# Kernel tuning notes

Measured on AMD Instinct MI355X. Metric: run time of the kernel, lower is better.

## Reference

```python
import jax, jax.numpy as jnp
import numpy as np

B, N_SERIES, T, HIDDEN = 256, 512, 512, 1024
EPS = 1e-5  # BatchNorm1d default eps


def setup_inputs() -> dict:
    key = jax.random.key(0)
    ks = jax.random.split(key, 6)
    s_in = 1.0 / np.sqrt(N_SERIES)
    s_hid = 1.0 / np.sqrt(2 * HIDDEN)
    s_out = 1.0 / np.sqrt(HIDDEN)
    return {
        "x": jax.random.normal(ks[0], (B, N_SERIES, T), dtype=jnp.float32),
        # input_layer: Linear(n_series -> hidden)
        "Wi": jax.random.uniform(ks[1], (HIDDEN, N_SERIES), jnp.float32, -s_in, s_in),
        "bi": jnp.zeros((HIDDEN,), jnp.float32),
        # hidden_layer: Linear(2*hidden -> hidden)
        "Wh": jax.random.uniform(ks[2], (HIDDEN, 2 * HIDDEN), jnp.float32, -s_hid, s_hid),
        "bh": jnp.zeros((HIDDEN,), jnp.float32),
        # BatchNorm1d(hidden) affine params
        "gamma": jnp.ones((HIDDEN,), jnp.float32),
        "beta": jnp.zeros((HIDDEN,), jnp.float32),
        # last_layer: Linear(hidden -> n_series)
        "Wl": jax.random.uniform(ks[3], (N_SERIES, HIDDEN), jnp.float32, -s_out, s_out),
        "bl": jnp.zeros((N_SERIES,), jnp.float32),
    }


def reference(x, Wi, bi, Wh, bh, gamma, beta, Wl, bl):
    # x: [B, n_series, T] -> time-major [T, B, n_series]
    xt = jnp.transpose(x, (2, 0, 1))
    h0 = jnp.zeros((x.shape[0], Wh.shape[0]), x.dtype)

    def step(h, x_t):
        inp = x_t @ Wi.T + bi                              # [B, H]
        emb = jnp.concatenate([inp, h], axis=1)            # [B, 2H]
        h_new = jnp.tanh(emb @ Wh.T + bh)                  # [B, H]
        return h_new, None

    hidden, _ = jax.lax.scan(step, h0, xt)
    # BatchNorm1d, training-mode batch statistics (biased variance)
    mean = jnp.mean(hidden, axis=0)
    var = jnp.var(hidden, axis=0)
    h_bn = gamma * (hidden - mean) / jnp.sqrt(var + EPS) + beta
    return h_bn @ Wl.T + bl                                # [B, n_series]
```

## Files before the change

kernel.cpp:

```cpp
#include <hip/hip_runtime.h>

typedef _Float16 f16;
typedef _Float16 half8 __attribute__((ext_vector_type(8)));
typedef float f32x4 __attribute__((ext_vector_type(4)));

#define HIDDEN 1024
#define NSER 512
#define BATCH 256
#define TSTEPS 512

__device__ __forceinline__ float tanh_fast(float x) {
  x = fminf(15.0f, fmaxf(-15.0f, x));
  float e = __expf(2.0f * x);
  return (e - 1.0f) / (e + 1.0f);
}


__global__ __launch_bounds__(256) void convert_whl_kernel(const float* __restrict__ Wh,
                                                          f16* __restrict__ WhLh) {
  int idx = blockIdx.x * 256 + threadIdx.x;
  int j = idx >> 10, k = idx & 1023;
  WhLh[idx] = (f16)Wh[((size_t)j << 11) + k];
}

__global__ __launch_bounds__(256) void convert_wl_kernel(const float* __restrict__ Wl,
                                                         f16* __restrict__ Wlh) {
  int idx = blockIdx.x * 256 + threadIdx.x;
  Wlh[idx] = (f16)Wl[idx];
}

__global__ __launch_bounds__(256) void transpose_wi_kernel(const float* __restrict__ Wi,
                                                           f16* __restrict__ WiT) {
  __shared__ float tile[32][33];
  int tx = threadIdx.x & 31, ty = threadIdx.x >> 5;
  int c0 = blockIdx.x * 32;
  int r0 = blockIdx.y * 32;
#pragma unroll
  for (int i = 0; i < 32; i += 8)
    tile[ty + i][tx] = Wi[(size_t)(r0 + ty + i) * NSER + c0 + tx];
  __syncthreads();
#pragma unroll
  for (int i = 0; i < 32; i += 8)
    WiT[(size_t)(c0 + ty + i) * HIDDEN + r0 + tx] = (f16)tile[tx][ty + i];
}

__global__ __launch_bounds__(256) void transpose_x_kernel(const float* __restrict__ x,
                                                          f16* __restrict__ xT) {
  __shared__ float tile[32][33];
  int b = blockIdx.z;
  int t0 = blockIdx.x * 32, n0 = blockIdx.y * 32;
  int tx = threadIdx.x & 31, ty = threadIdx.x >> 5;
#pragma unroll
  for (int i = 0; i < 32; i += 8)
    tile[ty + i][tx] = x[((size_t)b * NSER + n0 + ty + i) * TSTEPS + t0 + tx];
  __syncthreads();
#pragma unroll
  for (int i = 0; i < 32; i += 8)
    xT[((size_t)(t0 + ty + i) * BATCH + b) * NSER + n0 + tx] = (f16)tile[tx][ty + i];
}

__global__ __launch_bounds__(256) void beff_kernel(const float* __restrict__ Wh,
                                                   const float* __restrict__ bi,
                                                   const float* __restrict__ bh,
                                                   float* __restrict__ beff) {
  __shared__ float red[256];
  int j = blockIdx.x;
  float s = 0.f;
  for (int k = threadIdx.x; k < HIDDEN; k += 256)
    s += Wh[(size_t)j * 2048 + k] * bi[k];
  red[threadIdx.x] = s;
  __syncthreads();
  for (int off = 128; off > 0; off >>= 1) {
    if (threadIdx.x < (unsigned)off) red[threadIdx.x] += red[threadIdx.x + off];
    __syncthreads();
  }
  if (threadIdx.x == 0) beff[j] = bh[j] + red[0];
}

template <bool OUT_F16, bool HAS_BIAS>
__global__ __launch_bounds__(256) void gemm_f16_kernel(const f16* __restrict__ A,
                                                       const f16* __restrict__ B,
                                                       const float* __restrict__ bias,
                                                       void* __restrict__ Cp,
                                                       int M, int N, int K) {
  (void)M;
  __shared__ f16 As[128 * 64];
  __shared__ f16 Bs[128 * 64];
  const int tid = threadIdx.x;
  const int l = tid & 63, w = tid >> 6;
  const int wr = w >> 1, wc = w & 1;
  const int lr = l & 15, lg = l >> 4;
  const size_t m0 = (size_t)blockIdx.y * 128, n0 = (size_t)blockIdx.x * 128;
  f32x4 acc[4][4] = {};
  for (int k0 = 0; k0 < K; k0 += 64) {
    half8 ar[4], br[4];
#pragma unroll
    for (int c = 0; c < 4; ++c) {
      int Gq = c * 256 + tid;
      int row = Gq >> 3, colg = Gq & 7;
      ar[c] = *(const half8*)&A[(m0 + row) * K + k0 + colg * 8];
      br[c] = *(const half8*)&B[(n0 + row) * K + k0 + colg * 8];
    }
    __syncthreads();
#pragma unroll
    for (int c = 0; c < 4; ++c) {
      int Gq = c * 256 + tid;
      *(half8*)&As[Gq * 8] = ar[c];
      *(half8*)&Bs[Gq * 8] = br[c];
    }
    __syncthreads();
#pragma unroll
    for (int ks = 0; ks < 2; ++ks) {
      half8 a[4], b[4];
#pragma unroll
      for (int i = 0; i < 4; ++i)
        a[i] = *(const half8*)&As[(wr * 64 + i * 16 + lr) * 64 + ks * 32 + lg * 8];
#pragma unroll
      for (int i = 0; i < 4; ++i)
        b[i] = *(const half8*)&Bs[(wc * 64 + i * 16 + lr) * 64 + ks * 32 + lg * 8];
#pragma unroll
      for (int mi = 0; mi < 4; ++mi)
#pragma unroll
        for (int ni = 0; ni < 4; ++ni)
          acc[mi][ni] = __builtin_amdgcn_mfma_f32_16x16x32_f16(a[mi], b[ni], acc[mi][ni], 0, 0, 0);
    }
  }
#pragma unroll
  for (int mi = 0; mi < 4; ++mi) {
#pragma unroll
    for (int ni = 0; ni < 4; ++ni) {
      size_t n = n0 + wc * 64 + ni * 16 + lr;
      float bv = 0.f;
      if constexpr (HAS_BIAS) bv = bias[n];
#pragma unroll
      for (int r = 0; r < 4; ++r) {
        size_t m = m0 + wr * 64 + mi * 16 + lg * 4 + r;
        float v = acc[mi][ni][r] + bv;
        if constexpr (OUT_F16)
          ((f16*)Cp)[m * (size_t)N + n] = (f16)v;
        else
          ((float*)Cp)[m * (size_t)N + n] = v;
      }
    }
  }
}

__global__ __launch_bounds__(512) void rnn_kernel(const float* __restrict__ Wh,
                                                  const f16* __restrict__ Z,
                                                  f16* hb0, f16* hb1,
                                                  float* __restrict__ h_final,
                                                  unsigned int* canary) {
  const int bid = blockIdx.x;
  const int g = bid >> 3, q = bid & 7;
  const int tid = threadIdx.x;
  const int l = tid & 63, w = tid >> 6;
  const int lr = l & 15, lg = l >> 4;
  const int b0 = g * 16;
  const int jcol = q * 128 + w * 16 + lr;

  half8 breg[32];
#pragma unroll
  for (int ks = 0; ks < 32; ++ks) {
    const float* s = &Wh[(size_t)jcol * 2048 + HIDDEN + ks * 32 + lg * 8];
    half8 hv;
#pragma unroll
    for (int i = 0; i < 8; ++i) hv[i] = (f16)s[i];
    breg[ks] = hv;
  }

  __shared__ f16 hs[16 * HIDDEN];

  for (int t = 0; t < TSTEPS; ++t) {
    const f16* hprev = (t & 1) ? hb1 : hb0;
    f16* hnext = (t & 1) ? hb0 : hb1;

    const f16* zp = &Z[((size_t)t * BATCH + b0 + lg * 4) * HIDDEN + jcol];
    f16 z0 = zp[0], z1 = zp[HIDDEN], z2 = zp[2 * HIDDEN], z3 = zp[3 * HIDDEN];

    {
      const unsigned* cp = &canary[g * 8 + (l & 7)];
      unsigned cv;
      int guard = 0;
      do {
        asm volatile("global_load_dword %0, %1, off sc0 sc1\n\ts_waitcnt vmcnt(0)"
                     : "=v"(cv)
                     : "v"(cp)
                     : "memory");
      } while (__ballot(cv < (unsigned)t) != 0ull && ++guard < (1 << 20));
    }

    half8 hv[4];
#pragma unroll
    for (int i = 0; i < 4; ++i) {
      int G = i * 512 + tid;
      int row = G >> 7, gI = G & 127;
      const f16* src = &hprev[(size_t)(b0 + row) * HIDDEN + gI * 8];
      asm volatile("global_load_dwordx4 %0, %1, off sc0 sc1" : "=v"(hv[i]) : "v"(src));
    }
    asm volatile("s_waitcnt vmcnt(0)" ::: "memory");

#pragma unroll
    for (int i = 0; i < 4; ++i) {
      int G = i * 512 + tid;
      int row = G >> 7, gI = G & 127;
      *(half8*)&hs[row * HIDDEN + ((gI ^ (row & 7)) * 8)] = hv[i];
    }
    __syncthreads();

    f32x4 acc0 = {0.f, 0.f, 0.f, 0.f}, acc1 = acc0, acc2 = acc0, acc3 = acc0;
#pragma unroll
    for (int ks = 0; ks < 32; ks += 4) {
      int gA0 = ks * 4 + lg;
      half8 a0 = *(const half8*)&hs[lr * HIDDEN + ((gA0 ^ (lr & 7)) * 8)];
      half8 a1 = *(const half8*)&hs[lr * HIDDEN + (((gA0 + 4) ^ (lr & 7)) * 8)];
      half8 a2 = *(const half8*)&hs[lr * HIDDEN + (((gA0 + 8) ^ (lr & 7)) * 8)];
      half8 a3 = *(const half8*)&hs[lr * HIDDEN + (((gA0 + 12) ^ (lr & 7)) * 8)];
      acc0 = __builtin_amdgcn_mfma_f32_16x16x32_f16(a0, breg[ks + 0], acc0, 0, 0, 0);
      acc1 = __builtin_amdgcn_mfma_f32_16x16x32_f16(a1, breg[ks + 1], acc1, 0, 0, 0);
      acc2 = __builtin_amdgcn_mfma_f32_16x16x32_f16(a2, breg[ks + 2], acc2, 0, 0, 0);
      acc3 = __builtin_amdgcn_mfma_f32_16x16x32_f16(a3, breg[ks + 3], acc3, 0, 0, 0);
    }
    f32x4 acc = (acc0 + acc1) + (acc2 + acc3);

    float v0 = tanh_fast(acc[0] + (float)z0);
    float v1 = tanh_fast(acc[1] + (float)z1);
    float v2 = tanh_fast(acc[2] + (float)z2);
    float v3 = tanh_fast(acc[3] + (float)z3);

    if (t == TSTEPS - 1) {
      h_final[(size_t)(b0 + lg * 4 + 0) * HIDDEN + jcol] = v0;
      h_final[(size_t)(b0 + lg * 4 + 1) * HIDDEN + jcol] = v1;
      h_final[(size_t)(b0 + lg * 4 + 2) * HIDDEN + jcol] = v2;
      h_final[(size_t)(b0 + lg * 4 + 3) * HIDDEN + jcol] = v3;
    } else {
      unsigned s0 = (unsigned)__builtin_bit_cast(unsigned short, (f16)v0);
      unsigned s1 = (unsigned)__builtin_bit_cast(unsigned short, (f16)v1);
      unsigned s2 = (unsigned)__builtin_bit_cast(unsigned short, (f16)v2);
      unsigned s3 = (unsigned)__builtin_bit_cast(unsigned short, (f16)v3);
      f16* p0 = &hnext[(size_t)(b0 + lg * 4 + 0) * HIDDEN + jcol];
      asm volatile("global_store_short %0, %1, off sc0 sc1" ::"v"(p0), "v"(s0) : "memory");
      asm volatile("global_store_short %0, %1, off sc0 sc1" ::"v"(p0 + HIDDEN), "v"(s1) : "memory");
      asm volatile("global_store_short %0, %1, off sc0 sc1" ::"v"(p0 + 2 * HIDDEN), "v"(s2) : "memory");
      asm volatile("global_store_short %0, %1, off sc0 sc1" ::"v"(p0 + 3 * HIDDEN), "v"(s3) : "memory");
      asm volatile("s_waitcnt vmcnt(0)" ::: "memory");
      __syncthreads();
      if (tid == 0) {
        unsigned nv = (unsigned)(t + 1);
        asm volatile("global_store_dword %0, %1, off sc0 sc1" ::"v"(&canary[g * 8 + q]),
                     "v"(nv)
                     : "memory");
      }
    }
  }
}

__global__ __launch_bounds__(256) void bn_kernel(const float* __restrict__ hf,
                                                 const float* __restrict__ gamma,
                                                 const float* __restrict__ beta,
                                                 f16* __restrict__ hbn) {
  int j = blockIdx.x * 256 + threadIdx.x;
  float s1 = 0.f, s2 = 0.f;
  for (int b = 0; b < BATCH; ++b) {
    float v = hf[(size_t)b * HIDDEN + j];
    s1 += v;
    s2 += v * v;
  }
  float mean = s1 * (1.f / BATCH);
  float var = s2 * (1.f / BATCH) - mean * mean;
  float sc = gamma[j] * rsqrtf(var + 1e-5f);
  float sh = beta[j] - mean * sc;
  for (int b = 0; b < BATCH; ++b)
    hbn[(size_t)b * HIDDEN + j] = (f16)(hf[(size_t)b * HIDDEN + j] * sc + sh);
}

extern "C" void kernel_launch(void* const* d_in, const int* in_sizes, int n_in,
                              void* d_out, int out_size, void* d_ws, size_t ws_size,
                              hipStream_t stream) {
  (void)in_sizes; (void)n_in; (void)out_size;
  const float* x     = (const float*)d_in[0];
  const float* Wi    = (const float*)d_in[1];
  const float* bi    = (const float*)d_in[2];
  const float* Wh    = (const float*)d_in[3];
  const float* bh    = (const float*)d_in[4];
  const float* gamma = (const float*)d_in[5];
  const float* beta  = (const float*)d_in[6];
  const float* Wl    = (const float*)d_in[7];
  const float* bl    = (const float*)d_in[8];
  float* out = (float*)d_out;

  char* wsp = (char*)d_ws;
  size_t off = 0;
  auto alloc = [&](size_t bytes) -> void* {
    void* p = (void*)(wsp + off);
    off += (bytes + 255) & ~(size_t)255;
    return p;
  };
  f16*      Zb    = (f16*)alloc((size_t)TSTEPS * BATCH * HIDDEN * 2);
  f16*      xT    = (f16*)alloc((size_t)TSTEPS * BATCH * NSER * 2);
  f16*      WhLh  = (f16*)alloc((size_t)HIDDEN * HIDDEN * 2);
  f16*      WiT   = (f16*)alloc((size_t)NSER * HIDDEN * 2);
  f16*      Wlh   = (f16*)alloc((size_t)NSER * HIDDEN * 2);
  f16*      Weff  = (f16*)alloc((size_t)HIDDEN * NSER * 2);
  float*    beff  = (float*)alloc(HIDDEN * 4);
  f16*      hbuf0 = (f16*)alloc((size_t)BATCH * HIDDEN * 2);
  f16*      hbuf1 = (f16*)alloc((size_t)BATCH * HIDDEN * 2);
  float*    hfin  = (float*)alloc((size_t)BATCH * HIDDEN * 4);
  f16*      hbn   = (f16*)alloc((size_t)BATCH * HIDDEN * 2);
  unsigned* canary = (unsigned*)alloc(16 * 8 * 4);
  if (off > ws_size) return;

  hipMemsetAsync(canary, 0, 16 * 8 * 4, stream);
  hipMemsetAsync(hbuf0, 0, (size_t)BATCH * HIDDEN * 2, stream);

  convert_whl_kernel<<<4096, 256, 0, stream>>>(Wh, WhLh);
  transpose_wi_kernel<<<dim3(16, 32), 256, 0, stream>>>(Wi, WiT);
  convert_wl_kernel<<<2048, 256, 0, stream>>>(Wl, Wlh);
  beff_kernel<<<1024, 256, 0, stream>>>(Wh, bi, bh, beff);
  gemm_f16_kernel<true, false><<<dim3(4, 8), 256, 0, stream>>>(WhLh, WiT, nullptr, Weff,
                                                               1024, NSER, HIDDEN);
  transpose_x_kernel<<<dim3(16, 16, 256), 256, 0, stream>>>(x, xT);
  gemm_f16_kernel<true, true><<<dim3(8, 1024), 256, 0, stream>>>(xT, Weff, beff, Zb,
                                                                 TSTEPS * BATCH, HIDDEN, NSER);
  rnn_kernel<<<128, 512, 0, stream>>>(Wh, Zb, hbuf0, hbuf1, hfin, canary);
  bn_kernel<<<4, 256, 0, stream>>>(hfin, gamma, beta, hbn);
  gemm_f16_kernel<false, true><<<dim3(4, 2), 256, 0, stream>>>(hbn, Wlh, bl, out,
                                                               BATCH, NSER, HIDDEN);
}
```

Before: 2.794 ms.

## Replace canary flag sync with tagged-data mailboxes in persistent RNN kernel

Each hidden-state value is now written as a 32-bit word carrying the fp16 value plus a timestep tag, so consumers poll the data itself instead of spinning on a separate canary counter and then reloading h. This removes the store-drain, the block barrier and the flag-write round trip on every step, and also prefetches the next step's Z values during the current step. In exchange the mailbox traffic doubles in size, the spin loop rereads the full 16-row tile on each miss, and it relies on 32-bit stores being seen whole.

```diff
diff --git a/kernel.cpp b/kernel.cpp
--- a/kernel.cpp
+++ b/kernel.cpp
@@ -3,6 +3,8 @@
 typedef _Float16 f16;
 typedef _Float16 half8 __attribute__((ext_vector_type(8)));
 typedef float f32x4 __attribute__((ext_vector_type(4)));
+typedef unsigned int u32x4 __attribute__((ext_vector_type(4)));
+typedef unsigned int u32x2 __attribute__((ext_vector_type(2)));
 
 #define HIDDEN 1024
 #define NSER 512
@@ -145,11 +147,10 @@
   }
 }
 
-__global__ __launch_bounds__(512) void rnn_kernel(const float* __restrict__ Wh,
-                                                  const f16* __restrict__ Z,
-                                                  f16* hb0, f16* hb1,
-                                                  float* __restrict__ h_final,
-                                                  unsigned int* canary) {
+__global__ __launch_bounds__(512, 2) void rnn_kernel(const float* __restrict__ Wh,
+                                                     const f16* __restrict__ Z,
+                                                     unsigned* mb0, unsigned* mb1,
+                                                     float* __restrict__ h_final) {
   const int bid = blockIdx.x;
   const int g = bid >> 3, q = bid & 7;
   const int tid = threadIdx.x;
@@ -158,6 +159,9 @@
   const int b0 = g * 16;
   const int jcol = q * 128 + w * 16 + lr;
 
+  const int u = tid & 255;
+  const int rb = tid >> 8;
+
   half8 breg[32];
 #pragma unroll
   for (int ks = 0; ks < 32; ++ks) {
@@ -170,42 +174,71 @@
 
   __shared__ f16 hs[16 * HIDDEN];
 
-  for (int t = 0; t < TSTEPS; ++t) {
-    const f16* hprev = (t & 1) ? hb1 : hb0;
-    f16* hnext = (t & 1) ? hb0 : hb1;
-
-    const f16* zp = &Z[((size_t)t * BATCH + b0 + lg * 4) * HIDDEN + jcol];
-    f16 z0 = zp[0], z1 = zp[HIDDEN], z2 = zp[2 * HIDDEN], z3 = zp[3 * HIDDEN];
-
+  __builtin_amdgcn_sched_barrier(0);
+  asm volatile("s_waitcnt vmcnt(0)" ::: "memory");
+
+  unsigned zA[4], zB[4];
+  {
+    const f16* zp = &Z[((size_t)0 * BATCH + b0 + lg * 4) * HIDDEN + jcol];
+#pragma unroll
+    for (int r = 0; r < 4; ++r)
+      asm volatile("global_load_ushort %0, %1, off" : "=v"(zA[r]) : "v"(zp + r * HIDDEN));
+  }
+
+  auto step = [&](int t, unsigned (&zc)[4], unsigned (&zn)[4]) {
+    const unsigned* mbr = (t & 1) ? mb1 : mb0;
+    unsigned* mbw = (t & 1) ? mb0 : mb1;
+
+    u32x4 hv[8];
+#pragma unroll
+    for (int i = 0; i < 8; ++i) {
+      const unsigned* src = mbr + (size_t)(b0 + i * 2 + rb) * HIDDEN + u * 4;
+      asm volatile("global_load_dwordx4 %0, %1, off sc0 sc1" : "=v"(hv[i]) : "v"(src));
+    }
     {
-      const unsigned* cp = &canary[g * 8 + (l & 7)];
-      unsigned cv;
-      int guard = 0;
-      do {
-        asm volatile("global_load_dword %0, %1, off sc0 sc1\n\ts_waitcnt vmcnt(0)"
-                     : "=v"(cv)
-                     : "v"(cp)
-                     : "memory");
-      } while (__ballot(cv < (unsigned)t) != 0ull && ++guard < (1 << 20));
-    }
-
-    half8 hv[4];
-#pragma unroll
-    for (int i = 0; i < 4; ++i) {
-      int G = i * 512 + tid;
-      int row = G >> 7, gI = G & 127;
-      const f16* src = &hprev[(size_t)(b0 + row) * HIDDEN + gI * 8];
-      asm volatile("global_load_dwordx4 %0, %1, off sc0 sc1" : "=v"(hv[i]) : "v"(src));
-    }
-    asm volatile("s_waitcnt vmcnt(0)" ::: "memory");
-
-#pragma unroll
-    for (int i = 0; i < 4; ++i) {
-      int G = i * 512 + tid;
-      int row = G >> 7, gI = G & 127;
-      *(half8*)&hs[row * HIDDEN + ((gI ^ (row & 7)) * 8)] = hv[i];
-    }
-    __syncthreads();
+      int tp = (t + 1 < TSTEPS) ? t + 1 : TSTEPS - 1;
+      const f16* zp = &Z[((size_t)tp * BATCH + b0 + lg * 4) * HIDDEN + jcol];
+#pragma unroll
+      for (int r = 0; r < 4; ++r)
+        asm volatile("global_load_ushort %0, %1, off" : "=v"(zn[r]) : "v"(zp + r * HIDDEN));
+    }
+    asm volatile("s_waitcnt vmcnt(4)" ::: "memory");
+
+    const unsigned texp = (unsigned)t << 16;
+    int tries = 0;
+    while (true) {
+      unsigned bad = 0;
+#pragma unroll
+      for (int i = 0; i < 8; ++i) {
+        bad |= hv[i][0] ^ texp;
+        bad |= hv[i][1] ^ texp;
+        bad |= hv[i][2] ^ texp;
+        bad |= hv[i][3] ^ texp;
+      }
+      if (__ballot((bad >> 16) != 0u) == 0ull) break;
+      if (++tries > (1 << 18)) break;
+#pragma unroll
+      for (int i = 0; i < 8; ++i) {
+        const unsigned* src = mbr + (size_t)(b0 + i * 2 + rb) * HIDDEN + u * 4;
+        asm volatile("global_load_dwordx4 %0, %1, off sc0 sc1" : "=v"(hv[i]) : "v"(src));
+      }
+      asm volatile("s_waitcnt vmcnt(0)" ::: "memory");
+    }
+
+#pragma unroll
+    for (int i = 0; i < 8; ++i) {
+      asm volatile("" : "+v"(hv[i]));
+      unsigned p0 = (hv[i][0] & 0xffffu) | (hv[i][1] << 16);
+      unsigned p1 = (hv[i][2] & 0xffffu) | (hv[i][3] << 16);
+      int row = i * 2 + rb;
+      int gI = u >> 1, half = u & 1;
+      u32x2 pv = {p0, p1};
+      *(u32x2*)((char*)hs + row * 2048 + ((gI ^ (row & 7)) * 16) + half * 8) = pv;
+    }
+    asm volatile("s_waitcnt lgkmcnt(0)" ::: "memory");
+    __builtin_amdgcn_sched_barrier(0);
+    __builtin_amdgcn_s_barrier();
+    __builtin_amdgcn_sched_barrier(0);
 
     f32x4 acc0 = {0.f, 0.f, 0.f, 0.f}, acc1 = acc0, acc2 = acc0, acc3 = acc0;
 #pragma unroll
@@ -222,10 +255,12 @@
     }
     f32x4 acc = (acc0 + acc1) + (acc2 + acc3);
 
-    float v0 = tanh_fast(acc[0] + (float)z0);
-    float v1 = tanh_fast(acc[1] + (float)z1);
-    float v2 = tanh_fast(acc[2] + (float)z2);
-    float v3 = tanh_fast(acc[3] + (float)z3);
+#pragma unroll
+    for (int r = 0; r < 4; ++r) asm volatile("" : "+v"(zc[r]));
+    float v0 = tanh_fast(acc[0] + (float)__builtin_bit_cast(f16, (unsigned short)zc[0]));
+    float v1 = tanh_fast(acc[1] + (float)__builtin_bit_cast(f16, (unsigned short)zc[1]));
+    float v2 = tanh_fast(acc[2] + (float)__builtin_bit_cast(f16, (unsigned short)zc[2]));
+    float v3 = tanh_fast(acc[3] + (float)__builtin_bit_cast(f16, (unsigned short)zc[3]));
 
     if (t == TSTEPS - 1) {
       h_final[(size_t)(b0 + lg * 4 + 0) * HIDDEN + jcol] = v0;
@@ -233,24 +268,25 @@
       h_final[(size_t)(b0 + lg * 4 + 2) * HIDDEN + jcol] = v2;
       h_final[(size_t)(b0 + lg * 4 + 3) * HIDDEN + jcol] = v3;
     } else {
-      unsigned s0 = (unsigned)__builtin_bit_cast(unsigned short, (f16)v0);
-      unsigned s1 = (unsigned)__builtin_bit_cast(unsigned short, (f16)v1);
-      unsigned s2 = (unsigned)__builtin_bit_cast(unsigned short, (f16)v2);
-      unsigned s3 = (unsigned)__builtin_bit_cast(unsigned short, (f16)v3);
-      f16* p0 = &hnext[(size_t)(b0 + lg * 4 + 0) * HIDDEN + jcol];
-      asm volatile("global_store_short %0, %1, off sc0 sc1" ::"v"(p0), "v"(s0) : "memory");
-      asm volatile("global_store_short %0, %1, off sc0 sc1" ::"v"(p0 + HIDDEN), "v"(s1) : "memory");
-      asm volatile("global_store_short %0, %1, off sc0 sc1" ::"v"(p0 + 2 * HIDDEN), "v"(s2) : "memory");
-      asm volatile("global_store_short %0, %1, off sc0 sc1" ::"v"(p0 + 3 * HIDDEN), "v"(s3) : "memory");
-      asm volatile("s_waitcnt vmcnt(0)" ::: "memory");
-      __syncthreads();
-      if (tid == 0) {
-        unsigned nv = (unsigned)(t + 1);
-        asm volatile("global_store_dword %0, %1, off sc0 sc1" ::"v"(&canary[g * 8 + q]),
-                     "v"(nv)
-                     : "memory");
-      }
-    }
+      const unsigned tag = (unsigned)(t + 1) << 16;
+      unsigned d0 = (unsigned)__builtin_bit_cast(unsigned short, (f16)v0) | tag;
+      unsigned d1 = (unsigned)__builtin_bit_cast(unsigned short, (f16)v1) | tag;
+      unsigned d2 = (unsigned)__builtin_bit_cast(unsigned short, (f16)v2) | tag;
+      unsigned d3 = (unsigned)__builtin_bit_cast(unsigned short, (f16)v3) | tag;
+      unsigned* p0 = mbw + (size_t)(b0 + lg * 4) * HIDDEN + jcol;
+      asm volatile("global_store_dword %0, %1, off sc0 sc1" ::"v"(p0), "v"(d0) : "memory");
+      asm volatile("global_store_dword %0, %1, off sc0 sc1" ::"v"(p0 + HIDDEN), "v"(d1) : "memory");
+      asm volatile("global_store_dword %0, %1, off sc0 sc1" ::"v"(p0 + 2 * HIDDEN), "v"(d2) : "memory");
+      asm volatile("global_store_dword %0, %1, off sc0 sc1" ::"v"(p0 + 3 * HIDDEN), "v"(d3) : "memory");
+    }
+    __builtin_amdgcn_sched_barrier(0);
+    __builtin_amdgcn_s_barrier();
+    __builtin_amdgcn_sched_barrier(0);
+  };
+
+  for (int t = 0; t < TSTEPS; t += 2) {
+    step(t, zA, zB);
+    step(t + 1, zB, zA);
   }
 }
 
@@ -302,15 +338,14 @@
   f16*      Wlh   = (f16*)alloc((size_t)NSER * HIDDEN * 2);
   f16*      Weff  = (f16*)alloc((size_t)HIDDEN * NSER * 2);
   float*    beff  = (float*)alloc(HIDDEN * 4);
-  f16*      hbuf0 = (f16*)alloc((size_t)BATCH * HIDDEN * 2);
-  f16*      hbuf1 = (f16*)alloc((size_t)BATCH * HIDDEN * 2);
+  unsigned* mb0   = (unsigned*)alloc((size_t)BATCH * HIDDEN * 4);
+  unsigned* mb1   = (unsigned*)alloc((size_t)BATCH * HIDDEN * 4);
   float*    hfin  = (float*)alloc((size_t)BATCH * HIDDEN * 4);
   f16*      hbn   = (f16*)alloc((size_t)BATCH * HIDDEN * 2);
-  unsigned* canary = (unsigned*)alloc(16 * 8 * 4);
   if (off > ws_size) return;
 
-  hipMemsetAsync(canary, 0, 16 * 8 * 4, stream);
-  hipMemsetAsync(hbuf0, 0, (size_t)BATCH * HIDDEN * 2, stream);
+  hipMemsetAsync(mb0, 0, (size_t)BATCH * HIDDEN * 4, stream);
+  hipMemsetAsync(mb1, 0, (size_t)BATCH * HIDDEN * 4, stream);
 
   convert_whl_kernel<<<4096, 256, 0, stream>>>(Wh, WhLh);
   transpose_wi_kernel<<<dim3(16, 32), 256, 0, stream>>>(Wi, WiT);
@@ -321,7 +356,7 @@
   transpose_x_kernel<<<dim3(16, 16, 256), 256, 0, stream>>>(x, xT);
   gemm_f16_kernel<true, true><<<dim3(8, 1024), 256, 0, stream>>>(xT, Weff, beff, Zb,
                                                                  TSTEPS * BATCH, HIDDEN, NSER);
-  rnn_kernel<<<128, 512, 0, stream>>>(Wh, Zb, hbuf0, hbuf1, hfin, canary);
+  rnn_kernel<<<128, 512, 0, stream>>>(Wh, Zb, mb0, mb1, hfin);
   bn_kernel<<<4, 256, 0, stream>>>(hfin, gamma, beta, hbn);
   gemm_f16_kernel<false, true><<<dim3(4, 2), 256, 0, stream>>>(hbn, Wlh, bl, out,
                                                                BATCH, NSER, HIDDEN);
```

Result: slower. 3.136 ms (+12.2%).

## Use 1024-thread RNN blocks with per-step atomic counter barrier across 4 blocks

Applied to the files above, without the earlier changes.

Each batch group of 16 rows is now handled by 4 blocks of 1024 threads instead of 8 blocks of 512, which halves the number of blocks that must synchronise every timestep. The per-block canary flags, polled before each step, are replaced by a per-(group,timestep) atomic counter. Each block increments it after storing its slice of h and spins until all 4 blocks have arrived. The aim is to cut inter-block synchronisation latency on the serial recurrence. The cost is 1024-thread blocks with 32 half8 weight registers per thread, which raises register pressure, and a relaxed-atomic spin whose memory ordering relies on the sc0 sc1 stores.

```diff
diff --git a/kernel.cpp b/kernel.cpp
--- a/kernel.cpp
+++ b/kernel.cpp
@@ -3,6 +3,7 @@
 typedef _Float16 f16;
 typedef _Float16 half8 __attribute__((ext_vector_type(8)));
 typedef float f32x4 __attribute__((ext_vector_type(4)));
+typedef unsigned int u32x4 __attribute__((ext_vector_type(4)));
 
 #define HIDDEN 1024
 #define NSER 512
@@ -145,18 +146,18 @@
   }
 }
 
-__global__ __launch_bounds__(512) void rnn_kernel(const float* __restrict__ Wh,
-                                                  const f16* __restrict__ Z,
-                                                  f16* hb0, f16* hb1,
-                                                  float* __restrict__ h_final,
-                                                  unsigned int* canary) {
+__global__ __launch_bounds__(1024) void rnn_kernel(const float* __restrict__ Wh,
+                                                   const f16* __restrict__ Z,
+                                                   f16* hb0, f16* hb1,
+                                                   float* __restrict__ h_final,
+                                                   unsigned int* cnt) {
   const int bid = blockIdx.x;
-  const int g = bid >> 3, q = bid & 7;
+  const int g = bid >> 2, q = bid & 3;
   const int tid = threadIdx.x;
   const int l = tid & 63, w = tid >> 6;
   const int lr = l & 15, lg = l >> 4;
   const int b0 = g * 16;
-  const int jcol = q * 128 + w * 16 + lr;
+  const int jcol = q * 256 + w * 16 + lr;
 
   half8 breg[32];
 #pragma unroll
@@ -177,22 +178,10 @@
     const f16* zp = &Z[((size_t)t * BATCH + b0 + lg * 4) * HIDDEN + jcol];
     f16 z0 = zp[0], z1 = zp[HIDDEN], z2 = zp[2 * HIDDEN], z3 = zp[3 * HIDDEN];
 
-    {
-      const unsigned* cp = &canary[g * 8 + (l & 7)];
-      unsigned cv;
-      int guard = 0;
-      do {
-        asm volatile("global_load_dword %0, %1, off sc0 sc1\n\ts_waitcnt vmcnt(0)"
-                     : "=v"(cv)
-                     : "v"(cp)
-                     : "memory");
-      } while (__ballot(cv < (unsigned)t) != 0ull && ++guard < (1 << 20));
-    }
-
-    half8 hv[4];
-#pragma unroll
-    for (int i = 0; i < 4; ++i) {
-      int G = i * 512 + tid;
+    half8 hv[2];
+#pragma unroll
+    for (int i = 0; i < 2; ++i) {
+      int G = i * 1024 + tid;
       int row = G >> 7, gI = G & 127;
       const f16* src = &hprev[(size_t)(b0 + row) * HIDDEN + gI * 8];
       asm volatile("global_load_dwordx4 %0, %1, off sc0 sc1" : "=v"(hv[i]) : "v"(src));
@@ -200,8 +189,8 @@
     asm volatile("s_waitcnt vmcnt(0)" ::: "memory");
 
 #pragma unroll
-    for (int i = 0; i < 4; ++i) {
-      int G = i * 512 + tid;
+    for (int i = 0; i < 2; ++i) {
+      int G = i * 1024 + tid;
       int row = G >> 7, gI = G & 127;
       *(half8*)&hs[row * HIDDEN + ((gI ^ (row & 7)) * 8)] = hv[i];
     }
@@ -237,19 +226,22 @@
       unsigned s1 = (unsigned)__builtin_bit_cast(unsigned short, (f16)v1);
       unsigned s2 = (unsigned)__builtin_bit_cast(unsigned short, (f16)v2);
       unsigned s3 = (unsigned)__builtin_bit_cast(unsigned short, (f16)v3);
-      f16* p0 = &hnext[(size_t)(b0 + lg * 4 + 0) * HIDDEN + jcol];
+      f16* p0 = &hnext[(size_t)(b0 + lg * 4) * HIDDEN + jcol];
       asm volatile("global_store_short %0, %1, off sc0 sc1" ::"v"(p0), "v"(s0) : "memory");
       asm volatile("global_store_short %0, %1, off sc0 sc1" ::"v"(p0 + HIDDEN), "v"(s1) : "memory");
       asm volatile("global_store_short %0, %1, off sc0 sc1" ::"v"(p0 + 2 * HIDDEN), "v"(s2) : "memory");
       asm volatile("global_store_short %0, %1, off sc0 sc1" ::"v"(p0 + 3 * HIDDEN), "v"(s3) : "memory");
       asm volatile("s_waitcnt vmcnt(0)" ::: "memory");
       __syncthreads();
-      if (tid == 0) {
-        unsigned nv = (unsigned)(t + 1);
-        asm volatile("global_store_dword %0, %1, off sc0 sc1" ::"v"(&canary[g * 8 + q]),
-                     "v"(nv)
-                     : "memory");
+      if (tid == 0)
+        __hip_atomic_fetch_add(&cnt[g * TSTEPS + t], 1u, __ATOMIC_RELAXED,
+                               __HIP_MEMORY_SCOPE_AGENT);
+      int guard = 0;
+      while (__hip_atomic_load(&cnt[g * TSTEPS + t], __ATOMIC_RELAXED,
+                               __HIP_MEMORY_SCOPE_AGENT) < 4u) {
+        if (++guard > (1 << 20)) break;
       }
+      asm volatile("" ::: "memory");
     }
   }
 }
@@ -306,10 +298,10 @@
   f16*      hbuf1 = (f16*)alloc((size_t)BATCH * HIDDEN * 2);
   float*    hfin  = (float*)alloc((size_t)BATCH * HIDDEN * 4);
   f16*      hbn   = (f16*)alloc((size_t)BATCH * HIDDEN * 2);
-  unsigned* canary = (unsigned*)alloc(16 * 8 * 4);
+  unsigned* cnt   = (unsigned*)alloc(16 * TSTEPS * 4);
   if (off > ws_size) return;
 
-  hipMemsetAsync(canary, 0, 16 * 8 * 4, stream);
+  hipMemsetAsync(cnt, 0, 16 * TSTEPS * 4, stream);
   hipMemsetAsync(hbuf0, 0, (size_t)BATCH * HIDDEN * 2, stream);
 
   convert_whl_kernel<<<4096, 256, 0, stream>>>(Wh, WhLh);
@@ -321,7 +313,7 @@
   transpose_x_kernel<<<dim3(16, 16, 256), 256, 0, stream>>>(x, xT);
   gemm_f16_kernel<true, true><<<dim3(8, 1024), 256, 0, stream>>>(xT, Weff, beff, Zb,
                                                                  TSTEPS * BATCH, HIDDEN, NSER);
-  rnn_kernel<<<128, 512, 0, stream>>>(Wh, Zb, hbuf0, hbuf1, hfin, canary);
+  rnn_kernel<<<64, 1024, 0, stream>>>(Wh, Zb, hbuf0, hbuf1, hfin, cnt);
   bn_kernel<<<4, 256, 0, stream>>>(hfin, gamma, beta, hbn);
   gemm_f16_kernel<false, true><<<dim3(4, 2), 256, 0, stream>>>(hbn, Wlh, bl, out,
                                                                BATCH, NSER, HIDDEN);
```

New measurement: 6.415 ms. +129.6%, slower.
